# Kernel optimization log

Measured on AMD Instinct MI355X. Metric: run time of the kernel, lower is better.

The kernel has to match this reference:

```python
import jax, jax.numpy as jnp
import numpy as np

DIM, HEADS, HDIM, B, L = 2048, 16, 128, 2, 2048

def setup_inputs() -> dict:
    key = jax.random.key(0)
    ks = jax.random.split(key, 7)
    s = 1.0 / np.sqrt(DIM)
    return {
        "x": jax.random.normal(ks[0], (B, L, DIM), jnp.float32),
        "rope_emb": jax.random.uniform(ks[1], (L, HDIM), jnp.float32),
        "wq": jax.random.normal(ks[2], (DIM, DIM), jnp.float32) * s,
        "wk": jax.random.normal(ks[3], (DIM, DIM), jnp.float32) * s,
        "wv": jax.random.normal(ks[4], (DIM, DIM), jnp.float32) * s,
        "wo": jax.random.normal(ks[5], (DIM, DIM), jnp.float32) * s,
        "bo": jnp.zeros((DIM,), jnp.float32),
    }

def _rotate_half(x):
    x1, x2 = jnp.split(x, 2, axis=-1)
    return jnp.concatenate((-x2, x1), axis=-1)

def reference(x, rope_emb, wq, wk, wv, wo, bo):
    Bq, Lq, D = x.shape
    # projections; torch Linear: y = x @ W.T, weights here stored as [out,in]
    q = jnp.einsum("bld,ed->ble", x, wq).reshape(Bq, Lq, HEADS, HDIM).transpose(0, 2, 1, 3)
    k = jnp.einsum("bld,ed->ble", x, wk).reshape(Bq, Lq, HEADS, HDIM).transpose(0, 2, 1, 3)
    v = jnp.einsum("bld,ed->ble", x, wv).reshape(Bq, Lq, HEADS, HDIM).transpose(0, 2, 1, 3)
    cos = jnp.cos(rope_emb)[None, None]  # [1,1,L,hd]
    sin = jnp.sin(rope_emb)[None, None]
    q = q * cos + _rotate_half(q) * sin
    k = k * cos + _rotate_half(k) * sin
    scale = HDIM ** -0.5
    attn = jnp.einsum("bhqd,bhkd->bhqk", q, k) * scale
    attn = jax.nn.softmax(attn, axis=-1)
    out = jnp.einsum("bhqk,bhkd->bhqd", attn, v)
    out = out.transpose(0, 2, 1, 3).reshape(Bq, Lq, D)
    return jnp.einsum("bld,ed->ble", out, wo) + bo
```

## Files before the change

kernel.cpp:

```cpp
#include <hip/hip_runtime.h>
#include <hip/hip_bf16.h>
#include <stdint.h>

#define DIMS  2048
#define HEADS 16
#define HD    128
#define BATCH 2
#define SEQ   2048
#define MROWS (BATCH*SEQ)
#define QKVN  (3*DIMS)

using bf16x8 = __attribute__((ext_vector_type(8))) short;
using f32x4  = __attribute__((ext_vector_type(4))) float;
using f32x16 = __attribute__((ext_vector_type(16))) float;
using u16x4  = __attribute__((ext_vector_type(4))) unsigned short;

__device__ __forceinline__ unsigned short f2b(float f){
    __hip_bfloat16 h = __float2bfloat16(f);
    return *reinterpret_cast<unsigned short*>(&h);
}
__device__ __forceinline__ float b2f(unsigned short u){
    __hip_bfloat16 h;
    *reinterpret_cast<unsigned short*>(&h) = u;
    return __bfloat162float(h);
}
__device__ __forceinline__ unsigned int pkbf(float lo, float hi){
    return (unsigned int)f2b(lo) | ((unsigned int)f2b(hi) << 16);
}

__device__ __forceinline__ void glds16(const void* g, void* l){
    __builtin_amdgcn_global_load_lds(
        (const __attribute__((address_space(1))) unsigned int*)g,
        (__attribute__((address_space(3))) unsigned int*)l, 16, 0, 0);
}


__global__ void k_prep(const float* __restrict__ x,
                       const float* __restrict__ w0, const float* __restrict__ w1,
                       const float* __restrict__ w2, const float* __restrict__ w3,
                       const float* __restrict__ rope,
                       unsigned short* __restrict__ x_bf,
                       unsigned short* __restrict__ d0, unsigned short* __restrict__ d1,
                       unsigned short* __restrict__ d2, unsigned short* __restrict__ d3,
                       float* __restrict__ ct, float* __restrict__ st){
    const int y = blockIdx.y;
    if (y == 6){
        const int i = blockIdx.x*blockDim.x + threadIdx.x;
        if (i >= SEQ*HD) return;
        const float v = rope[i];
        ct[i] = cosf(v);
        st[i] = sinf(v);
        return;
    }
    const float* src;
    unsigned short* dst;
    size_t off = 0;
    if      (y == 0){ src = w0; dst = d0; }
    else if (y == 1){ src = w1; dst = d1; }
    else if (y == 2){ src = w2; dst = d2; }
    else if (y == 3){ src = w3; dst = d3; }
    else            { src = x;  dst = x_bf; off = (size_t)(y - 4) * 1048576; }
    const size_t i = off + blockIdx.x*blockDim.x + threadIdx.x;
    const float4 v = reinterpret_cast<const float4*>(src)[i];
    u16x4 o = { f2b(v.x), f2b(v.y), f2b(v.z), f2b(v.w) };
    *reinterpret_cast<u16x4*>(dst + 4*i) = o;
}


__global__ void k_kropevt(unsigned short* __restrict__ qkv,
                          const float* __restrict__ ct, const float* __restrict__ st,
                          unsigned short* __restrict__ vt){
    __shared__ unsigned short t[64*68];
    const int bid = blockIdx.x;
    if (bid < 2048){
        const int idx = bid*blockDim.x + threadIdx.x;
        const int d0 = (idx & 7) << 3;
        const int h  = (idx >> 3) & (HEADS-1);
        const int l  = (idx >> 7) & (SEQ-1);
        const int b  = idx >> 18;
        const float4* cp = reinterpret_cast<const float4*>(ct + l*HD + d0);
        const float4* sp = reinterpret_cast<const float4*>(st + l*HD + d0);
        const float4 cl0 = cp[0],  cl1 = cp[1];
        const float4 sl0 = sp[0],  sl1 = sp[1];
        const float4 cu0 = cp[16], cu1 = cp[17];
        const float4 su0 = sp[16], su1 = sp[17];
        const float cl[8] = {cl0.x,cl0.y,cl0.z,cl0.w, cl1.x,cl1.y,cl1.z,cl1.w};
        const float sl[8] = {sl0.x,sl0.y,sl0.z,sl0.w, sl1.x,sl1.y,sl1.z,sl1.w};
        const float cu[8] = {cu0.x,cu0.y,cu0.z,cu0.w, cu1.x,cu1.y,cu1.z,cu1.w};
        const float su[8] = {su0.x,su0.y,su0.z,su0.w, su1.x,su1.y,su1.z,su1.w};
        unsigned short* rp = qkv + (size_t)(b*SEQ + l)*QKVN + DIMS + h*HD + d0;
        bf16x8 lo = *reinterpret_cast<const bf16x8*>(rp);
        bf16x8 hi = *reinterpret_cast<const bf16x8*>(rp + 64);
        bf16x8 olo, ohi;
        #pragma unroll
        for (int j = 0; j < 8; ++j){
            const float x1 = b2f((unsigned short)lo[j]);
            const float x2 = b2f((unsigned short)hi[j]);
            olo[j] = (short)f2b(x1*cl[j] - x2*sl[j]);
            ohi[j] = (short)f2b(x2*cu[j] + x1*su[j]);
        }
        *reinterpret_cast<bf16x8*>(rp)      = olo;
        *reinterpret_cast<bf16x8*>(rp + 64) = ohi;
        return;
    }
    const int bid2 = bid - 2048;
    const int lt = bid2 & 31;
    const int dt = (bid2 >> 5) & 1;
    const int bh = bid2 >> 6;
    const int b = bh >> 4, h = bh & 15;
    const int tid = threadIdx.x;
    const int l0 = lt << 6;
    #pragma unroll
    for (int it = 0; it < 4; ++it){
        const int c = tid + (it<<8);
        const int l = c >> 4;
        const int d4 = (c & 15) << 2;
        const u16x4 v = *reinterpret_cast<const u16x4*>(
            qkv + (size_t)(b*SEQ + l0 + l)*QKVN + 2*DIMS + h*HD + (dt<<6) + d4);
        *reinterpret_cast<u16x4*>(&t[l*68 + d4]) = v;
    }
    __syncthreads();
    #pragma unroll
    for (int it = 0; it < 4; ++it){
        const int c = tid + (it<<8);
        const int d = c >> 4;
        const int l4 = (c & 15) << 2;
        u16x4 o = { t[(l4+0)*68 + d], t[(l4+1)*68 + d], t[(l4+2)*68 + d], t[(l4+3)*68 + d] };
        *reinterpret_cast<u16x4*>(&vt[((size_t)bh*HD + (dt<<6) + d)*SEQ + l0 + l4]) = o;
    }
}


template<int FINAL>
__global__ __launch_bounds__(256) void k_gemm_bt(
    const unsigned short* __restrict__ A, const unsigned short* __restrict__ B,
    void* __restrict__ C, const float* __restrict__ bias, int M, int N, int K)
{
    __shared__ unsigned short lA[128*64];
    __shared__ unsigned short lB[128*64];
    const int tid  = threadIdx.x;
    const int lane = tid & 63;
    const int wave = tid >> 6;

    const int nbx = N >> 7;
    const int nwg = gridDim.x;
    const int cpx = nwg >> 3;
    const int bid = blockIdx.x;
    const int wg  = (bid & 7)*cpx + (bid >> 3);
    const int m0 = (wg / nbx) << 7;
    const int n0 = (wg % nbx) << 7;

    const int wr = (wave >> 1) << 6;
    const int wc = (wave & 1) << 6;

    f32x4 acc[4][4] = {};

    const int srow_base = (wave<<3) + (lane>>3);
    const int schunk = lane & 7;

    for (int k0 = 0; k0 < K; k0 += 64){
        #pragma unroll
        for (int i = 0; i < 4; ++i){
            const int row  = (i<<5) + srow_base;
            const int scol = k0 + ((schunk ^ (row & 7)) << 3);
            glds16(A + (size_t)(m0 + row)*K + scol, &lA[((i<<5) + (wave<<3)) << 6]);
            glds16(B + (size_t)(n0 + row)*K + scol, &lB[((i<<5) + (wave<<3)) << 6]);
        }
        __syncthreads();
        #pragma unroll
        for (int ks = 0; ks < 2; ++ks){
            bf16x8 af[4], bfr[4];
            const int colbase = (ks<<5) + ((lane>>4)<<3);
            #pragma unroll
            for (int mi = 0; mi < 4; ++mi){
                const int row = wr + (mi<<4) + (lane & 15);
                af[mi] = *reinterpret_cast<const bf16x8*>(&lA[(row<<6) + (colbase ^ ((row&7)<<3))]);
            }
            #pragma unroll
            for (int ni = 0; ni < 4; ++ni){
                const int row = wc + (ni<<4) + (lane & 15);
                bfr[ni] = *reinterpret_cast<const bf16x8*>(&lB[(row<<6) + (colbase ^ ((row&7)<<3))]);
            }
            #pragma unroll
            for (int mi = 0; mi < 4; ++mi)
                #pragma unroll
                for (int ni = 0; ni < 4; ++ni)
                    acc[mi][ni] = __builtin_amdgcn_mfma_f32_16x16x32_bf16(af[mi], bfr[ni], acc[mi][ni], 0, 0, 0);
        }
        __syncthreads();
    }

    const int r0 = (lane >> 4) << 2;
    const int cn = lane & 15;
    #pragma unroll
    for (int mi = 0; mi < 4; ++mi)
        #pragma unroll
        for (int r = 0; r < 4; ++r){
            const int gm = m0 + wr + (mi<<4) + r0 + r;
            #pragma unroll
            for (int ni = 0; ni < 4; ++ni){
                const int gn = n0 + wc + (ni<<4) + cn;
                const float v = acc[mi][ni][r];
                if (FINAL)
                    reinterpret_cast<float*>(C)[(size_t)gm*N + gn] = v + bias[gn];
                else
                    reinterpret_cast<unsigned short*>(C)[(size_t)gm*N + gn] = f2b(v);
            }
        }
}


union U8 { unsigned int w[4]; bf16x8 v; };

__global__ __launch_bounds__(256, 2) void k_attn(
    const unsigned short* __restrict__ qkv, const unsigned short* __restrict__ vt,
    const float* __restrict__ ct, const float* __restrict__ st,
    unsigned short* __restrict__ aout)
{
    __shared__ unsigned short smem[32768];

    const int tid  = threadIdx.x;
    const int lane = tid & 63;
    const int wave = tid >> 6;
    const int lq   = lane & 31;
    const int hi   = lane >> 5;
    const int bh = blockIdx.y;
    const int b = bh >> 4, h = bh & 15;
    const int q0w = (blockIdx.x << 7) + (wave << 5);

    const unsigned short* Kb = qkv + (size_t)b*SEQ*QKVN + DIMS + h*HD;
    const unsigned short* Vb = vt + (size_t)bh*HD*SEQ;

    bf16x8 qf[8];
    {
        const float qscale = 0.08838834764831845f * 1.4426950408889634f;
        const int l = q0w + lq;
        const unsigned short* qp = qkv + (size_t)(b*SEQ + l)*QKVN + h*HD + (hi<<3);
        #pragma unroll
        for (int ks = 0; ks < 8; ++ks)
            qf[ks] = *reinterpret_cast<const bf16x8*>(qp + (ks<<4));
        #pragma unroll
        for (int ks = 0; ks < 4; ++ks){
            const int d0 = (ks<<4) + (hi<<3);
            const float4 c0 = *reinterpret_cast<const float4*>(ct + l*HD + d0);
            const float4 c1 = *reinterpret_cast<const float4*>(ct + l*HD + d0 + 4);
            const float4 s0 = *reinterpret_cast<const float4*>(st + l*HD + d0);
            const float4 s1 = *reinterpret_cast<const float4*>(st + l*HD + d0 + 4);
            const float4 C0 = *reinterpret_cast<const float4*>(ct + l*HD + d0 + 64);
            const float4 C1 = *reinterpret_cast<const float4*>(ct + l*HD + d0 + 68);
            const float4 S0 = *reinterpret_cast<const float4*>(st + l*HD + d0 + 64);
            const float4 S1 = *reinterpret_cast<const float4*>(st + l*HD + d0 + 68);
            const float cl[8] = {c0.x,c0.y,c0.z,c0.w, c1.x,c1.y,c1.z,c1.w};
            const float sl[8] = {s0.x,s0.y,s0.z,s0.w, s1.x,s1.y,s1.z,s1.w};
            const float cu[8] = {C0.x,C0.y,C0.z,C0.w, C1.x,C1.y,C1.z,C1.w};
            const float su[8] = {S0.x,S0.y,S0.z,S0.w, S1.x,S1.y,S1.z,S1.w};
            #pragma unroll
            for (int j = 0; j < 8; ++j){
                const float x1 = b2f((unsigned short)qf[ks][j]);
                const float x2 = b2f((unsigned short)qf[ks+4][j]);
                qf[ks][j]   = (short)f2b((x1*cl[j] - x2*sl[j]) * qscale);
                qf[ks+4][j] = (short)f2b((x2*cu[j] + x1*su[j]) * qscale);
            }
        }
    }

    float m_run = -3e38f, l_run = 0.f;
    f32x16 oacc[4] = {};

    #define STAGE(pb, kv0) do { \
        _Pragma("unroll") \
        for (int i = 0; i < 4; ++i){ \
            const int kr = (wave<<4) + (i<<2) + (lane>>4); \
            glds16(Kb + (size_t)((kv0) + kr)*QKVN + (((lane&15) ^ (kr&7))<<3), \
                   &smem[((pb)<<13) + (((wave<<4) + (i<<2))<<7)]); \
            const int dr = (wave<<5) + (i<<3) + (lane>>3); \
            glds16(Vb + (size_t)dr*SEQ + (kv0) + (((lane&7) ^ (dr&7))<<3), \
                   &smem[16384 + ((pb)<<13) + (((wave<<5) + (i<<3))<<6)]); \
        } \
    } while(0)

    int buf = 0;
    STAGE(0, 0);
    __syncthreads();

    for (int t = 0; t < SEQ/64; ++t){
        if (t < SEQ/64 - 1) STAGE(buf^1, (t+1)*64);

        const unsigned short* Kbuf = &smem[buf<<13];
        const unsigned short* Vbuf = &smem[16384 + (buf<<13)];

        f32x16 st0 = {}, st1 = {};
        __builtin_amdgcn_s_setprio(1);
        #pragma unroll
        for (int ks = 0; ks < 8; ++ks){
            const int col = (((ks<<1) + hi) ^ (lq & 7)) << 3;
            bf16x8 k0 = *reinterpret_cast<const bf16x8*>(&Kbuf[(lq<<7) + col]);
            bf16x8 k1 = *reinterpret_cast<const bf16x8*>(&Kbuf[((32+lq)<<7) + col]);
            st0 = __builtin_amdgcn_mfma_f32_32x32x16_bf16(k0, qf[ks], st0, 0, 0, 0);
            st1 = __builtin_amdgcn_mfma_f32_32x32x16_bf16(k1, qf[ks], st1, 0, 0, 0);
        }
        __builtin_amdgcn_s_setprio(0);

        float tmax = st0[0];
        #pragma unroll
        for (int r = 1; r < 16; ++r) tmax = fmaxf(tmax, st0[r]);
        #pragma unroll
        for (int r = 0; r < 16; ++r) tmax = fmaxf(tmax, st1[r]);
        tmax = fmaxf(tmax, __shfl_xor(tmax, 32));

        const bool defer = __all(tmax <= m_run + 8.0f);
        if (!defer){
            const float mnew = fmaxf(m_run, tmax);
            const float al = __builtin_amdgcn_exp2f(m_run - mnew);
            m_run = mnew;
            l_run *= al;
            #pragma unroll
            for (int dt = 0; dt < 4; ++dt) oacc[dt] *= al;
        }
        float tsum = 0.f;
        #pragma unroll
        for (int r = 0; r < 16; ++r){ float p = __builtin_amdgcn_exp2f(st0[r] - m_run); st0[r] = p; tsum += p; }
        #pragma unroll
        for (int r = 0; r < 16; ++r){ float p = __builtin_amdgcn_exp2f(st1[r] - m_run); st1[r] = p; tsum += p; }
        tsum += __shfl_xor(tsum, 32);
        l_run += tsum;

        bf16x8 pf[4];
        #define MAKEPF(dA, dB, SV) do { \
            unsigned int a0 = pkbf(SV[0],SV[1]),  b0 = pkbf(SV[2],SV[3]); \
            unsigned int c0 = pkbf(SV[4],SV[5]),  d0 = pkbf(SV[6],SV[7]); \
            unsigned int a1 = pkbf(SV[8],SV[9]),  b1 = pkbf(SV[10],SV[11]); \
            unsigned int c1 = pkbf(SV[12],SV[13]),d1 = pkbf(SV[14],SV[15]); \
            asm("v_permlane32_swap_b32 %0, %1" : "+v"(a0), "+v"(c0)); \
            asm("v_permlane32_swap_b32 %0, %1" : "+v"(b0), "+v"(d0)); \
            asm("v_permlane32_swap_b32 %0, %1" : "+v"(a1), "+v"(c1)); \
            asm("v_permlane32_swap_b32 %0, %1" : "+v"(b1), "+v"(d1)); \
            U8 u; \
            u.w[0] = a0; u.w[1] = b0; u.w[2] = c0; u.w[3] = d0; dA = u.v; \
            u.w[0] = a1; u.w[1] = b1; u.w[2] = c1; u.w[3] = d1; dB = u.v; \
        } while(0)
        MAKEPF(pf[0], pf[1], st0);
        MAKEPF(pf[2], pf[3], st1);
        #undef MAKEPF

        __builtin_amdgcn_s_setprio(1);
        #pragma unroll
        for (int dt = 0; dt < 4; ++dt){
            const int rowv = (dt<<5) + lq;
            #pragma unroll
            for (int f = 0; f < 4; ++f){
                const int col = (((f<<1) + hi) ^ (lq & 7)) << 3;
                bf16x8 vf = *reinterpret_cast<const bf16x8*>(&Vbuf[(rowv<<6) + col]);
                oacc[dt] = __builtin_amdgcn_mfma_f32_32x32x16_bf16(vf, pf[f], oacc[dt], 0, 0, 0);
            }
        }
        __builtin_amdgcn_s_setprio(0);

        __syncthreads();
        buf ^= 1;
    }
    #undef STAGE

    const float rl = 1.0f / l_run;
    unsigned short* oL = smem + wave*(32*132);
    #pragma unroll
    for (int dt = 0; dt < 4; ++dt)
        #pragma unroll
        for (int g = 0; g < 4; ++g){
            u16x4 w = { f2b(oacc[dt][g*4+0]*rl), f2b(oacc[dt][g*4+1]*rl),
                        f2b(oacc[dt][g*4+2]*rl), f2b(oacc[dt][g*4+3]*rl) };
            *reinterpret_cast<u16x4*>(&oL[lq*132 + (dt<<5) + (hi<<2) + (g<<3)]) = w;
        }
    #pragma unroll
    for (int i = 0; i < 16; ++i){
        const int q = (i<<1) + hi;
        u16x4 w = *reinterpret_cast<const u16x4*>(&oL[q*132 + (lq<<2)]);
        *reinterpret_cast<u16x4*>(&aout[(size_t)(b*SEQ + q0w + q)*DIMS + h*HD + (lq<<2)]) = w;
    }
}


extern "C" void kernel_launch(void* const* d_in, const int* in_sizes, int n_in,
                              void* d_out, int out_size, void* d_ws, size_t ws_size,
                              hipStream_t stream)
{
    const float* x    = (const float*)d_in[0];
    const float* rope = (const float*)d_in[1];
    const float* wq   = (const float*)d_in[2];
    const float* wk   = (const float*)d_in[3];
    const float* wv   = (const float*)d_in[4];
    const float* wo   = (const float*)d_in[5];
    const float* bo   = (const float*)d_in[6];
    float* out = (float*)d_out;

    char* ws = (char*)d_ws;
    unsigned short* x_bf   = (unsigned short*)(ws + 0);
    unsigned short* wqkv   = (unsigned short*)(ws + 16777216);
    unsigned short* wo_bf  = (unsigned short*)(ws + 41943040);
    float*          cos_t  = (float*)(ws + 50331648);
    float*          sin_t  = (float*)(ws + 51380224);
    unsigned short* qkv    = (unsigned short*)(ws + 52428800);
    unsigned short* vt     = (unsigned short*)(ws + 16777216);
    unsigned short* a_out  = (unsigned short*)(ws + 0);

    k_prep<<<dim3(4096, 7), 256, 0, stream>>>(x, wq, wk, wv, wo, rope,
                                              x_bf, wqkv, wqkv + 4194304, wqkv + 8388608, wo_bf,
                                              cos_t, sin_t);

    k_gemm_bt<0><<<(MROWS/128)*(QKVN/128), 256, 0, stream>>>(x_bf, wqkv, qkv, nullptr, MROWS, QKVN, DIMS);

    k_kropevt<<<4096, 256, 0, stream>>>(qkv, cos_t, sin_t, vt);

    k_attn<<<dim3(SEQ/128, BATCH*HEADS), 256, 0, stream>>>(qkv, vt, cos_t, sin_t, a_out);

    k_gemm_bt<1><<<(MROWS/128)*(DIMS/128), 256, 0, stream>>>(a_out, wo_bf, out, bo, MROWS, DIMS, DIMS);
}
```

Before: 285.7 us.

## Fuse K RoPE and V transpose into QKV GEMM epilogue

Removes the separate RoPE/V-transpose kernel by doing the work in the QKV GEMM epilogue. Tiles in the V region write their output transposed straight into the vt buffer. Tiles in the K region stage results in LDS, apply RoPE, then store. The qkv buffer now holds only Q and K (row stride 4096), which saves a kernel launch and a read-modify-write pass over K and V, at the cost of a heavier epilogue and uncoalesced transposed stores for V.

```diff
diff --git a/kernel.cpp b/kernel.cpp
--- a/kernel.cpp
+++ b/kernel.cpp
@@ -9,6 +9,7 @@
 #define SEQ   2048
 #define MROWS (BATCH*SEQ)
 #define QKVN  (3*DIMS)
+#define QKP   4096
 
 using bf16x8 = __attribute__((ext_vector_type(8))) short;
 using f32x4  = __attribute__((ext_vector_type(4))) float;
@@ -67,77 +68,17 @@
 }
 
 
-__global__ void k_kropevt(unsigned short* __restrict__ qkv,
-                          const float* __restrict__ ct, const float* __restrict__ st,
-                          unsigned short* __restrict__ vt){
-    __shared__ unsigned short t[64*68];
-    const int bid = blockIdx.x;
-    if (bid < 2048){
-        const int idx = bid*blockDim.x + threadIdx.x;
-        const int d0 = (idx & 7) << 3;
-        const int h  = (idx >> 3) & (HEADS-1);
-        const int l  = (idx >> 7) & (SEQ-1);
-        const int b  = idx >> 18;
-        const float4* cp = reinterpret_cast<const float4*>(ct + l*HD + d0);
-        const float4* sp = reinterpret_cast<const float4*>(st + l*HD + d0);
-        const float4 cl0 = cp[0],  cl1 = cp[1];
-        const float4 sl0 = sp[0],  sl1 = sp[1];
-        const float4 cu0 = cp[16], cu1 = cp[17];
-        const float4 su0 = sp[16], su1 = sp[17];
-        const float cl[8] = {cl0.x,cl0.y,cl0.z,cl0.w, cl1.x,cl1.y,cl1.z,cl1.w};
-        const float sl[8] = {sl0.x,sl0.y,sl0.z,sl0.w, sl1.x,sl1.y,sl1.z,sl1.w};
-        const float cu[8] = {cu0.x,cu0.y,cu0.z,cu0.w, cu1.x,cu1.y,cu1.z,cu1.w};
-        const float su[8] = {su0.x,su0.y,su0.z,su0.w, su1.x,su1.y,su1.z,su1.w};
-        unsigned short* rp = qkv + (size_t)(b*SEQ + l)*QKVN + DIMS + h*HD + d0;
-        bf16x8 lo = *reinterpret_cast<const bf16x8*>(rp);
-        bf16x8 hi = *reinterpret_cast<const bf16x8*>(rp + 64);
-        bf16x8 olo, ohi;
-        #pragma unroll
-        for (int j = 0; j < 8; ++j){
-            const float x1 = b2f((unsigned short)lo[j]);
-            const float x2 = b2f((unsigned short)hi[j]);
-            olo[j] = (short)f2b(x1*cl[j] - x2*sl[j]);
-            ohi[j] = (short)f2b(x2*cu[j] + x1*su[j]);
-        }
-        *reinterpret_cast<bf16x8*>(rp)      = olo;
-        *reinterpret_cast<bf16x8*>(rp + 64) = ohi;
-        return;
-    }
-    const int bid2 = bid - 2048;
-    const int lt = bid2 & 31;
-    const int dt = (bid2 >> 5) & 1;
-    const int bh = bid2 >> 6;
-    const int b = bh >> 4, h = bh & 15;
-    const int tid = threadIdx.x;
-    const int l0 = lt << 6;
-    #pragma unroll
-    for (int it = 0; it < 4; ++it){
-        const int c = tid + (it<<8);
-        const int l = c >> 4;
-        const int d4 = (c & 15) << 2;
-        const u16x4 v = *reinterpret_cast<const u16x4*>(
-            qkv + (size_t)(b*SEQ + l0 + l)*QKVN + 2*DIMS + h*HD + (dt<<6) + d4);
-        *reinterpret_cast<u16x4*>(&t[l*68 + d4]) = v;
-    }
-    __syncthreads();
-    #pragma unroll
-    for (int it = 0; it < 4; ++it){
-        const int c = tid + (it<<8);
-        const int d = c >> 4;
-        const int l4 = (c & 15) << 2;
-        u16x4 o = { t[(l4+0)*68 + d], t[(l4+1)*68 + d], t[(l4+2)*68 + d], t[(l4+3)*68 + d] };
-        *reinterpret_cast<u16x4*>(&vt[((size_t)bh*HD + (dt<<6) + d)*SEQ + l0 + l4]) = o;
-    }
-}
-
-
-template<int FINAL>
+template<int MODE>
 __global__ __launch_bounds__(256) void k_gemm_bt(
     const unsigned short* __restrict__ A, const unsigned short* __restrict__ B,
-    void* __restrict__ C, const float* __restrict__ bias, int M, int N, int K)
+    void* __restrict__ C, const float* __restrict__ bias,
+    unsigned short* __restrict__ vt, const float* __restrict__ ct, const float* __restrict__ st,
+    int M, int N, int K, int ldc)
 {
-    __shared__ unsigned short lA[128*64];
-    __shared__ unsigned short lB[128*64];
+    __shared__ unsigned short sbuf[16896];
+    unsigned short* lA = sbuf;
+    unsigned short* lB = sbuf + 8192;
+
     const int tid  = threadIdx.x;
     const int lane = tid & 63;
     const int wave = tid >> 6;
@@ -192,21 +133,81 @@
 
     const int r0 = (lane >> 4) << 2;
     const int cn = lane & 15;
+
+    if (MODE == 1){
+        #pragma unroll
+        for (int mi = 0; mi < 4; ++mi)
+            #pragma unroll
+            for (int r = 0; r < 4; ++r){
+                const int gm = m0 + wr + (mi<<4) + r0 + r;
+                #pragma unroll
+                for (int ni = 0; ni < 4; ++ni){
+                    const int gn = n0 + wc + (ni<<4) + cn;
+                    reinterpret_cast<float*>(C)[(size_t)gm*ldc + gn] = acc[mi][ni][r] + bias[gn];
+                }
+            }
+        return;
+    }
+
+    const int region = n0 >> 11;
+    if (region == 2){
+        const int b   = m0 >> 11;
+        const int l0b = m0 & (SEQ-1);
+        const int hh  = (n0 - 2*DIMS) >> 7;
+        #pragma unroll
+        for (int mi = 0; mi < 4; ++mi){
+            const int l0 = l0b + wr + (mi<<4) + r0;
+            #pragma unroll
+            for (int ni = 0; ni < 4; ++ni){
+                const int d = wc + (ni<<4) + cn;
+                u16x4 w = { f2b(acc[mi][ni][0]), f2b(acc[mi][ni][1]),
+                            f2b(acc[mi][ni][2]), f2b(acc[mi][ni][3]) };
+                *reinterpret_cast<u16x4*>(
+                    &vt[(size_t)(((b<<4) + hh)*HD + d)*SEQ + l0]) = w;
+            }
+        }
+        return;
+    }
+    if (region == 0){
+        #pragma unroll
+        for (int mi = 0; mi < 4; ++mi)
+            #pragma unroll
+            for (int r = 0; r < 4; ++r){
+                const int gm = m0 + wr + (mi<<4) + r0 + r;
+                #pragma unroll
+                for (int ni = 0; ni < 4; ++ni){
+                    const int gn = n0 + wc + (ni<<4) + cn;
+                    reinterpret_cast<unsigned short*>(C)[(size_t)gm*ldc + gn] = f2b(acc[mi][ni][r]);
+                }
+            }
+        return;
+    }
     #pragma unroll
     for (int mi = 0; mi < 4; ++mi)
         #pragma unroll
         for (int r = 0; r < 4; ++r){
-            const int gm = m0 + wr + (mi<<4) + r0 + r;
-            #pragma unroll
-            for (int ni = 0; ni < 4; ++ni){
-                const int gn = n0 + wc + (ni<<4) + cn;
-                const float v = acc[mi][ni][r];
-                if (FINAL)
-                    reinterpret_cast<float*>(C)[(size_t)gm*N + gn] = v + bias[gn];
-                else
-                    reinterpret_cast<unsigned short*>(C)[(size_t)gm*N + gn] = f2b(v);
-            }
-        }
+            const int row = wr + (mi<<4) + r0 + r;
+            #pragma unroll
+            for (int ni = 0; ni < 4; ++ni)
+                sbuf[row*132 + wc + (ni<<4) + cn] = f2b(acc[mi][ni][r]);
+        }
+    __syncthreads();
+    unsigned short* Cq = (unsigned short*)C;
+    #pragma unroll
+    for (int it = 0; it < 32; ++it){
+        const int e  = (it<<8) + tid;
+        const int lr = e >> 6;
+        const int d  = e & 63;
+        const int gm = m0 + lr;
+        const int l  = gm & (SEQ-1);
+        const float x1 = b2f(sbuf[lr*132 + d]);
+        const float x2 = b2f(sbuf[lr*132 + d + 64]);
+        const float c0 = ct[l*HD + d],      s0 = st[l*HD + d];
+        const float c1 = ct[l*HD + d + 64], s1 = st[l*HD + d + 64];
+        unsigned short* rp = Cq + (size_t)gm*ldc + n0;
+        rp[d]      = f2b(x1*c0 - x2*s0);
+        rp[d + 64] = f2b(x2*c1 + x1*s1);
+    }
 }
 
 
@@ -228,14 +229,14 @@
     const int b = bh >> 4, h = bh & 15;
     const int q0w = (blockIdx.x << 7) + (wave << 5);
 
-    const unsigned short* Kb = qkv + (size_t)b*SEQ*QKVN + DIMS + h*HD;
+    const unsigned short* Kb = qkv + (size_t)b*SEQ*QKP + DIMS + h*HD;
     const unsigned short* Vb = vt + (size_t)bh*HD*SEQ;
 
     bf16x8 qf[8];
     {
         const float qscale = 0.08838834764831845f * 1.4426950408889634f;
         const int l = q0w + lq;
-        const unsigned short* qp = qkv + (size_t)(b*SEQ + l)*QKVN + h*HD + (hi<<3);
+        const unsigned short* qp = qkv + (size_t)(b*SEQ + l)*QKP + h*HD + (hi<<3);
         #pragma unroll
         for (int ks = 0; ks < 8; ++ks)
             qf[ks] = *reinterpret_cast<const bf16x8*>(qp + (ks<<4));
@@ -271,7 +272,7 @@
         _Pragma("unroll") \
         for (int i = 0; i < 4; ++i){ \
             const int kr = (wave<<4) + (i<<2) + (lane>>4); \
-            glds16(Kb + (size_t)((kv0) + kr)*QKVN + (((lane&15) ^ (kr&7))<<3), \
+            glds16(Kb + (size_t)((kv0) + kr)*QKP + (((lane&15) ^ (kr&7))<<3), \
                    &smem[((pb)<<13) + (((wave<<4) + (i<<2))<<7)]); \
             const int dr = (wave<<5) + (i<<3) + (lane>>3); \
             glds16(Vb + (size_t)dr*SEQ + (kv0) + (((lane&7) ^ (dr&7))<<3), \
@@ -400,18 +401,18 @@
     float*          cos_t  = (float*)(ws + 50331648);
     float*          sin_t  = (float*)(ws + 51380224);
     unsigned short* qkv    = (unsigned short*)(ws + 52428800);
-    unsigned short* vt     = (unsigned short*)(ws + 16777216);
+    unsigned short* vt     = (unsigned short*)(ws + 85983232);
     unsigned short* a_out  = (unsigned short*)(ws + 0);
 
     k_prep<<<dim3(4096, 7), 256, 0, stream>>>(x, wq, wk, wv, wo, rope,
                                               x_bf, wqkv, wqkv + 4194304, wqkv + 8388608, wo_bf,
                                               cos_t, sin_t);
 
-    k_gemm_bt<0><<<(MROWS/128)*(QKVN/128), 256, 0, stream>>>(x_bf, wqkv, qkv, nullptr, MROWS, QKVN, DIMS);
-
-    k_kropevt<<<4096, 256, 0, stream>>>(qkv, cos_t, sin_t, vt);
+    k_gemm_bt<0><<<(MROWS/128)*(QKVN/128), 256, 0, stream>>>(
+        x_bf, wqkv, qkv, nullptr, vt, cos_t, sin_t, MROWS, QKVN, DIMS, QKP);
 
     k_attn<<<dim3(SEQ/128, BATCH*HEADS), 256, 0, stream>>>(qkv, vt, cos_t, sin_t, a_out);
 
-    k_gemm_bt<1><<<(MROWS/128)*(DIMS/128), 256, 0, stream>>>(a_out, wo_bf, out, bo, MROWS, DIMS, DIMS);
-}
+    k_gemm_bt<1><<<(MROWS/128)*(DIMS/128), 256, 0, stream>>>(
+        a_out, wo_bf, out, bo, nullptr, nullptr, nullptr, MROWS, DIMS, DIMS, DIMS);
+}
```

New measurement: 289.2 us. About the same (+1.2%).
